# Performance work log

Hardware: AMD Instinct MI355X
Metric: run time of the kernel (lower is better)

Reference implementation:

```python
import math
import jax, jax.numpy as jnp
import numpy as np

N_NODES = 20000
N_EDGES = 320000
N_GRAPHS = 50
MAX_RADIUS = 3.5
NB = 8
NUM_NEIGHBORS = 16.0
NUM_NODES_TYP = 400.0
EPS = 1e-6
C_S = math.sin(math.pi / 8)
C_X = math.cos(math.pi / 8)
SQRT3 = math.sqrt(3.0)


def silu(x):
    return x * jax.nn.sigmoid(x)


def setup_inputs() -> dict:
    key = jax.random.key(0)
    ks = jax.random.split(key, 32)
    nrm = lambda i, s: jax.random.normal(ks[i], s, dtype=jnp.float32)
    return {
        'pos': nrm(0, (N_NODES, 3)),
        'atom_type': jax.random.randint(ks[1], (N_NODES,), 0, 20),
        'edge_src': jax.random.randint(ks[2], (N_EDGES,), 0, N_NODES),
        'edge_dst': jax.random.randint(ks[3], (N_EDGES,), 0, N_NODES),
        'batch': jnp.sort(jax.random.randint(ks[4], (N_NODES,), 0, N_GRAPHS)),
        'embed': nrm(5, (20, 8)),
        'w_tp0': nrm(6, (8, 8, 8)),
        'tpself_ss': nrm(7, (2, 64, 64, 64)),
        'tpself_vv': nrm(8, (2, 32, 32, 64)),
        'tpself_sv': nrm(9, (2, 64, 32, 32)),
        'tpself_vs': nrm(10, (2, 32, 64, 32)),
        'w_pen_ss': nrm(11, (64, 64, 16)),
        'w_pen_vv': nrm(12, (32, 32, 16)),
        'w_last': nrm(13, (16, 16, 1)),
        'sc0': nrm(14, (8, 96)),
        'lin1_0': nrm(15, (8, 8)),
        'fc0_w1': nrm(16, (NB, 64)),
        'fc0_w2': nrm(17, (64, 16)),
        'lin2_0s': nrm(18, (8, 96)),
        'lin2_0v': nrm(19, (8, 32)),
        'sc_s': nrm(20, (2, 64, 96)),
        'sc_v': nrm(21, (2, 32, 32)),
        'lin1_s': nrm(22, (2, 64, 64)),
        'lin1_v': nrm(23, (2, 32, 32)),
        'fc_w1': nrm(24, (2, NB, 64)),
        'fc_w2': nrm(25, (2, 64, 192)),
        'lin2_s': nrm(26, (2, 96, 96)),
        'lin2_v': nrm(27, (2, 96, 32)),
    }


def _edge_geometry(pos, edge_src, edge_dst):
    vec = pos[edge_src] - pos[edge_dst]            # [E,3]
    r = jnp.sqrt(jnp.sum(vec * vec, -1) + 1e-12)   # [E]
    r_safe = jnp.maximum(r, EPS)
    unit = vec / r_safe[:, None]
    sh0 = jnp.ones((vec.shape[0], 1), vec.dtype)   # Y_0 (component norm)
    sh1 = SQRT3 * unit                             # Y_1 (component norm)
    u = 2.0 * (r / MAX_RADIUS - 1.0)               # smooth_cutoff
    cut = 0.5 * (1.0 - jnp.cos(math.pi * u))
    cut = jnp.where(u > 0, 0.0, jnp.where(u < -1, 1.0, cut))
    ea_s = cut[:, None] * sh0
    ea_v = cut[:, None] * sh1
    n = jnp.arange(1, NB + 1, dtype=vec.dtype)     # bessel basis * sqrt(NB)
    basis = math.sqrt(2.0 / MAX_RADIUS) * jnp.sin(n[None] * math.pi * r_safe[:, None] / MAX_RADIUS) / r_safe[:, None]
    basis = basis * math.sqrt(NB)
    return ea_s, ea_v, basis


def _radial(basis, w1, w2):
    h = silu(basis @ w1 / math.sqrt(basis.shape[-1]))
    return h @ w2 / math.sqrt(w1.shape[-1])


def _tvnorm(ys, yv):
    ys = ys / jnp.sqrt(jnp.mean(ys * ys, -1, keepdims=True) + EPS)
    vn = jnp.mean(jnp.sum(yv * yv, -1), -1)
    return ys, yv / jnp.sqrt(vn + EPS)[:, None, None]


def _gate(ys, yv):
    return silu(ys[:, :64]), jax.nn.sigmoid(ys[:, 64:96])[:, :, None] * yv


def _tp_hidden(s, v, Wss, Wvv, Wsv, Wvs):
    a_s = 1.0 / math.sqrt(64 * 64 + 32 * 32)
    out_s = a_s * (jnp.einsum('ni,nj,ijk->nk', s, s, Wss)
                   + jnp.einsum('nic,njc,ijk->nk', v, v, Wvv) / SQRT3)
    a_v = 1.0 / math.sqrt(64 * 32 + 32 * 64)
    out_v = a_v * (jnp.einsum('ni,njc,ijk->nkc', s, v, Wsv)
                   + jnp.einsum('nic,nj,ijk->nkc', v, s, Wvs))
    return out_s, out_v


def _forward(pos, embed, w_tp0, tpself_ss, tpself_vv, tpself_sv, tpself_vs,
             w_pen_ss, w_pen_vv, w_last, sc0, lin1_0, fc0_w1, fc0_w2,
             lin2_0s, lin2_0v, sc_s, sc_v, lin1_s, lin1_v, fc_w1, fc_w2,
             lin2_s, lin2_v, atom_type, edge_src, edge_dst, batch):
    ea_s, ea_v, basis = _edge_geometry(pos, edge_src, edge_dst)
    inv_nn = 1.0 / math.sqrt(NUM_NEIGHBORS)

    x = embed[atom_type]                                    # [N,8]
    x = jnp.einsum('ni,nj,ijk->nk', x, x, w_tp0) / 8.0      # tp_self[0]

    # layer 0 convolution: 8x0e -> 96x0e + 32x1o
    sc_scal = x @ sc0 / math.sqrt(8)
    xl = x @ lin1_0 / math.sqrt(8)
    w = _radial(basis, fc0_w1, fc0_w2)                      # [E,16]
    xe = xl[edge_src]
    msg_s = w[:, :8] * xe * ea_s                            # 0e x 0e -> 0e
    msg_v = (w[:, 8:] * xe)[:, :, None] * ea_v[:, None, :]  # 0e x 1o -> 1o
    agg_s = jax.ops.segment_sum(msg_s, edge_dst, N_NODES) * inv_nn
    agg_v = jax.ops.segment_sum(msg_v, edge_dst, N_NODES) * inv_nn
    ys = C_S * sc_scal + C_X * (agg_s @ lin2_0s / math.sqrt(8))
    yv = jnp.einsum('nuc,uk->nkc', agg_v, lin2_0v) / math.sqrt(8)  # sc mask=0 here
    ys, yv = _tvnorm(ys, yv)
    s, v = _gate(ys, yv)                                    # [N,64],[N,32,3]

    # layers 1,2: residual with self tensor product
    for i in range(2):
        scs = s @ sc_s[i] / math.sqrt(64)
        scv = jnp.einsum('nuc,uk->nkc', v, sc_v[i]) / math.sqrt(32)
        ls = s @ lin1_s[i] / math.sqrt(64)
        lv = jnp.einsum('nuc,uk->nkc', v, lin1_v[i]) / math.sqrt(32)
        w = _radial(basis, fc_w1[i], fc_w2[i])              # [E,192]
        se, ve = ls[edge_src], lv[edge_src]
        m0 = w[:, :64] * se * ea_s                                    # 0e x 0e -> 0e
        m3 = w[:, 160:] * (jnp.sum(ve * ea_v[:, None, :], -1) / SQRT3)  # 1o x 1o -> 0e
        m1 = (w[:, 64:128] * se)[:, :, None] * ea_v[:, None, :]      # 0e x 1o -> 1o
        m2 = w[:, 128:160, None] * ve * ea_s[:, :, None]             # 1o x 0e -> 1o
        agg_s = jax.ops.segment_sum(jnp.concatenate([m0, m3], 1), edge_dst, N_NODES) * inv_nn
        agg_v = jax.ops.segment_sum(jnp.concatenate([m1, m2], 1), edge_dst, N_NODES) * inv_nn
        ys = C_S * scs + C_X * (agg_s @ lin2_s[i] / math.sqrt(96))
        yv = C_S * scv + C_X * (jnp.einsum('nuc,uk->nkc', agg_v, lin2_v[i]) / math.sqrt(96))
        ys, yv = _tvnorm(ys, yv)
        gs, gv = _gate(ys, yv)
        gs, gv = _tp_hidden(gs, gv, tpself_ss[i], tpself_vv[i], tpself_sv[i], tpself_vs[i])
        s = s + 0.1 * gs
        v = v + 0.1 * gv

    a_pen = 1.0 / math.sqrt(64 * 64 + 32 * 32)
    x16 = a_pen * (jnp.einsum('ni,nj,ijk->nk', s, s, w_pen_ss)
                   + jnp.einsum('nic,njc,ijk->nk', v, v, w_pen_vv) / SQRT3)
    x16 = silu(x16)
    out = jnp.einsum('ni,nj,ijo->no', x16, x16, w_last) / 16.0
    return jax.ops.segment_sum(out, batch, N_GRAPHS) / math.sqrt(NUM_NODES_TYP)


def reference(pos, embed, w_tp0, tpself_ss, tpself_vv, tpself_sv, tpself_vs,
              w_pen_ss, w_pen_vv, w_last, sc0, lin1_0, fc0_w1, fc0_w2,
              lin2_0s, lin2_0v, sc_s, sc_v, lin1_s, lin1_v, fc_w1, fc_w2,
              lin2_s, lin2_v, atom_type, edge_src, edge_dst, batch):
    return _forward(pos, embed, w_tp0, tpself_ss, tpself_vv, tpself_sv, tpself_vs,
                    w_pen_ss, w_pen_vv, w_last, sc0, lin1_0, fc0_w1, fc0_w2,
                    lin2_0s, lin2_0v, sc_s, sc_v, lin1_s, lin1_v, fc_w1, fc_w2,
                    lin2_s, lin2_v, atom_type, edge_src, edge_dst, batch)
```

## Files before the change

kernel.cpp:

```cpp
#include <hip/hip_runtime.h>
#include <math.h>

#define NN 20000
#define NE 320000
#define NG 50

#define INV_SQRT8  0.35355339059327373f
#define INV_SQRT32 0.17677669529663687f
#define INV_SQRT96 0.10206207261596575f
#define INV_NN     0.25f
#define CS_        0.3826834323650898f
#define CX_        0.9238795325112867f
#define SQRT3_     1.7320508075688772f
#define INV_SQRT3  0.5773502691896258f
#define A_S_       0.013975424859373686f
#define A_V_       0.015625f
#define PI_        3.14159265358979323846f

typedef __attribute__((ext_vector_type(8))) short bf16x8;
typedef __attribute__((ext_vector_type(4))) float f32x4;

__device__ __forceinline__ float siluf(float x) { return x / (1.0f + expf(-x)); }
__device__ __forceinline__ float sigmf(float x) { return 1.0f / (1.0f + expf(-x)); }

__device__ __forceinline__ void bsplit(float x, unsigned short& h, unsigned short& l) {
  unsigned int u = __float_as_uint(x);
  unsigned short hh = (unsigned short)((u + 0x7FFFu + ((u>>16)&1u))>>16);
  float fh = __uint_as_float(((unsigned int)hh)<<16);
  float r = x - fh;
  unsigned int u2 = __float_as_uint(r);
  unsigned short ll = (unsigned short)((u2 + 0x7FFFu + ((u2>>16)&1u))>>16);
  h = hh; l = ll;
}

__global__ __launch_bounds__(256) void k_hist(const int* __restrict__ edst, int* __restrict__ deg) {
  int e = blockIdx.x*256 + threadIdx.x;
  if (e < NE) atomicAdd(&deg[edst[e]], 1);
}

__global__ __launch_bounds__(256) void k_scan(const int* __restrict__ deg,
                                              int* __restrict__ rows, int* __restrict__ cursor) {
  __shared__ int buf[256];
  __shared__ int carry;
  int t = threadIdx.x;
  if (t == 0) { carry = 0; rows[0] = 0; }
  __syncthreads();
  for (int base = 0; base < NN; base += 256) {
    int i = base + t;
    int v = (i < NN) ? deg[i] : 0;
    buf[t] = v; __syncthreads();
    #pragma unroll
    for (int off = 1; off < 256; off <<= 1) {
      int x = (t >= off) ? buf[t-off] : 0;
      __syncthreads();
      buf[t] += x;
      __syncthreads();
    }
    int incl = buf[t] + carry;
    if (i < NN) { rows[i+1] = incl; cursor[i] = incl - v; }
    __syncthreads();
    if (t == 255) carry = incl;
    __syncthreads();
  }
}

__global__ __launch_bounds__(256) void k_scatter(const int* __restrict__ edst,
                                                 int* __restrict__ cursor, int* __restrict__ perm) {
  int e = blockIdx.x*256 + threadIdx.x;
  if (e >= NE) return;
  int p = atomicAdd(&cursor[edst[e]], 1);
  perm[p] = e;
}

__global__ __launch_bounds__(256) void k_geom(
    const float* __restrict__ pos, const int* __restrict__ esrc, const int* __restrict__ edst,
    const int* __restrict__ perm, int* __restrict__ esrc_s,
    float* __restrict__ ea_s, float* __restrict__ ea_v, float* __restrict__ basis) {
  int p = blockIdx.x*256 + threadIdx.x;
  if (p >= NE) return;
  int e = perm[p];
  int s = esrc[e], d = edst[e];
  esrc_s[p] = s;
  float vx = pos[3*s]   - pos[3*d];
  float vy = pos[3*s+1] - pos[3*d+1];
  float vz = pos[3*s+2] - pos[3*d+2];
  float r  = sqrtf(vx*vx + vy*vy + vz*vz + 1e-12f);
  float rs = fmaxf(r, 1e-6f);
  float inv = 1.0f / rs;
  float u = 2.0f*(r*(1.0f/3.5f) - 1.0f);
  float cut;
  if (u > 0.0f) cut = 0.0f;
  else if (u < -1.0f) cut = 1.0f;
  else cut = 0.5f*(1.0f - cosf(PI_*u));
  ea_s[p] = cut;
  float f = cut * SQRT3_ * inv;
  ea_v[p] = f*vx; ea_v[NE+p] = f*vy; ea_v[2*NE+p] = f*vz;
  const float cb = 2.1380899352993947f;
  #pragma unroll
  for (int n = 1; n <= 8; ++n)
    basis[(size_t)(n-1)*NE + p] = cb * sinf((float)n * (PI_/3.5f) * rs) * inv;
}

__global__ __launch_bounds__(256) void k_prep(
    const float* __restrict__ fc0_w1, const float* __restrict__ fc_w1,
    float* __restrict__ w1t) {
  int t = threadIdx.x;
  for (int idx = t; idx < 512; idx += 256) { int j = idx >> 3, k = idx & 7; w1t[idx] = fc0_w1[k*64 + j]; }
  for (int L = 0; L < 2; ++L)
    for (int idx = t; idx < 512; idx += 256) { int j = idx >> 3, k = idx & 7; w1t[512 + L*512 + idx] = fc_w1[L*512 + k*64 + j]; }
}

__global__ __launch_bounds__(256) void k_packw(
    const float* __restrict__ srcA, const float* __restrict__ srcB,
    unsigned short* __restrict__ dh, unsigned short* __restrict__ dl,
    int K, int N, int bound, float scA, float scB) {
  int idx = blockIdx.x*256 + threadIdx.x;
  if (idx >= K*N) return;
  int e = idx & 7;
  int lane = (idx >> 3) & 63;
  int rest = idx >> 9;
  int NT = N >> 4;
  int nt = rest % NT;
  int kt = rest / NT;
  int k = kt*32 + (lane>>4)*8 + e;
  int n = nt*16 + (lane&15);
  float w;
  if (k < bound) w = srcA[(size_t)k*N + n]*scA;
  else           w = srcB[(size_t)(k-bound)*N + n]*scB;
  unsigned short h, l;
  bsplit(w, h, l);
  dh[idx] = h; dl[idx] = l;
}

__global__ __launch_bounds__(256) void k_node0(
    const int* __restrict__ atype, const float* __restrict__ embed,
    const float* __restrict__ w_tp0, const float* __restrict__ sc0, const float* __restrict__ lin1_0,
    float* __restrict__ SC, float* __restrict__ LSB0) {
  int n = blockIdx.x*256 + threadIdx.x;
  if (n >= NN) return;
  int at = atype[n];
  float x[8];
  #pragma unroll
  for (int i = 0; i < 8; ++i) x[i] = embed[at*8 + i];
  float tc[8] = {0,0,0,0,0,0,0,0};
  #pragma unroll
  for (int i = 0; i < 8; ++i)
    #pragma unroll
    for (int j = 0; j < 8; ++j) {
      float p = x[i]*x[j];
      #pragma unroll
      for (int k = 0; k < 8; ++k) tc[k] += p * w_tp0[(i*8+j)*8 + k];
    }
  #pragma unroll
  for (int k = 0; k < 8; ++k) tc[k] *= 0.125f;
  #pragma unroll 1
  for (int k = 0; k < 96; ++k) {
    float a = 0.f;
    #pragma unroll
    for (int i = 0; i < 8; ++i) a += tc[i]*sc0[i*96+k];
    SC[(size_t)k*NN + n] = a * INV_SQRT8;
  }
  #pragma unroll
  for (int u = 0; u < 8; ++u) {
    float a = 0.f;
    #pragma unroll
    for (int i = 0; i < 8; ++i) a += tc[i]*lin1_0[i*8+u];
    LSB0[(size_t)n*8 + u] = a * INV_SQRT8;
  }
}

__global__ __launch_bounds__(256) void k_radial0(
    const float* __restrict__ BAS, const float* __restrict__ EAS,
    const float* __restrict__ w1t, const float* __restrict__ w2,
    float* __restrict__ RW, int pLo, int pHi, int cap) {
  __shared__ float tile[256*17];
  int t = threadIdx.x;
  int idx = blockIdx.x*256 + t;
  int p = pLo + idx;
  bool alive = p < pHi;
  float h[64];
  float es = 0.f;
  if (alive) {
    float b[8];
    #pragma unroll
    for (int k = 0; k < 8; ++k) b[k] = BAS[(size_t)k*NE + p];
    #pragma unroll
    for (int j = 0; j < 64; ++j) {
      float a = 0.f;
      #pragma unroll
      for (int k = 0; k < 8; ++k) a += b[k]*w1t[j*8+k];
      h[j] = siluf(a * INV_SQRT8);
    }
    es = EAS[p];
  }
  if (alive) {
    float acc[16] = {};
    #pragma unroll
    for (int j = 0; j < 64; ++j) {
      float hj = h[j];
      #pragma unroll
      for (int c = 0; c < 16; ++c) acc[c] += hj * w2[j*16 + c];
    }
    #pragma unroll
    for (int c = 0; c < 16; ++c) {
      float a = acc[c] * 0.125f;
      if (c < 8) a *= es;
      tile[t*17 + c] = a;
    }
  }
  __syncthreads();
  int e0 = blockIdx.x*256;
  #pragma unroll
  for (int i = 0; i < 16; ++i) {
    int lin = i*256 + t;
    int e = lin >> 4, c = lin & 15;
    if (pLo + e0 + e < pHi)
      RW[(size_t)(e0 + e)*16 + c] = tile[e*17 + c];
  }
}

__global__ __launch_bounds__(256) void k_radial(
    const float* __restrict__ BAS, const float* __restrict__ EAS,
    const float* __restrict__ w1t, const float* __restrict__ w2,
    float* __restrict__ RW, int pLo, int pHi, int cap) {
  __shared__ float tile[256*17];
  int t = threadIdx.x;
  int idx = blockIdx.x*256 + t;
  int p = pLo + idx;
  bool alive = p < pHi;
  float h[64];
  float es = 0.f;
  if (alive) {
    float b[8];
    #pragma unroll
    for (int k = 0; k < 8; ++k) b[k] = BAS[(size_t)k*NE + p];
    #pragma unroll
    for (int j = 0; j < 64; ++j) {
      float a = 0.f;
      #pragma unroll
      for (int k = 0; k < 8; ++k) a += b[k]*w1t[j*8+k];
      h[j] = siluf(a * INV_SQRT8);
    }
    es = EAS[p];
  }
  int e0 = blockIdx.x*256;
  int cc0 = blockIdx.y*3;
  #pragma unroll 1
  for (int ci = 0; ci < 3; ++ci) {
    int cc = cc0 + ci;
    if (alive) {
      float acc[16] = {};
      #pragma unroll
      for (int j = 0; j < 64; ++j) {
        float hj = h[j];
        const float* wr = w2 + j*192 + cc*16;
        #pragma unroll
        for (int c = 0; c < 16; ++c) acc[c] += hj * wr[c];
      }
      #pragma unroll
      for (int c = 0; c < 16; ++c) {
        int ch = cc*16 + c;
        float a = acc[c] * 0.125f;
        float f = (ch < 64) ? es : ((ch < 128) ? 1.0f : ((ch < 160) ? es : INV_SQRT3));
        tile[t*17 + c] = a*f;
      }
    }
    __syncthreads();
    #pragma unroll
    for (int i = 0; i < 16; ++i) {
      int lin = i*256 + t;
      int e = lin >> 4, c = lin & 15;
      if (pLo + e0 + e < pHi)
        RW[(size_t)(e0 + e)*192 + cc*16 + c] = tile[e*17 + c];
    }
    __syncthreads();
  }
}

__global__ __launch_bounds__(256) void k_gather0(
    const int* __restrict__ rows, const int* __restrict__ esrc_s,
    const float* __restrict__ EAV, const float* __restrict__ RW,
    const float* __restrict__ LSB0, float* __restrict__ AG0,
    int pLo, int pHi, int cap) {
  int t = blockIdx.x*256 + threadIdx.x;
  int d = t >> 3, u = t & 7;
  int lo = rows[d], hi = rows[d+1];
  lo = lo > pLo ? lo : pLo;
  hi = hi < pHi ? hi : pHi;
  if (lo >= hi) return;
  float aS = 0.f, a0 = 0.f, a1 = 0.f, a2 = 0.f;
  for (int p = lo; p < hi; ++p) {
    int q = p - pLo;
    int sn = esrc_s[p];
    float xe = LSB0[(size_t)sn*8 + u];
    const float* rwp = RW + (size_t)q*16;
    float r0 = rwp[u];
    float r1 = rwp[8+u];
    aS += r0*xe;
    float tt = r1*xe;
    a0 += tt*EAV[p]; a1 += tt*EAV[NE+p]; a2 += tt*EAV[2*NE+p];
  }
  float* ag = AG0 + (size_t)d*32;
  ag[u] += aS;
  ag[8 + u*3 + 0] += a0;
  ag[8 + u*3 + 1] += a1;
  ag[8 + u*3 + 2] += a2;
}

__global__ __launch_bounds__(256) void k_gather(
    const int* __restrict__ rows, const int* __restrict__ esrc_s,
    const float* __restrict__ EAS, const float* __restrict__ EAV,
    const float* __restrict__ RW, const float* __restrict__ LSB, const float* __restrict__ LVB,
    float* __restrict__ AG, int pLo, int pHi, int cap) {
  int gw = (blockIdx.x*256 + threadIdx.x) >> 6;
  int lane = threadIdx.x & 63;
  if (gw >= NN) return;
  int lo = rows[gw], hi = rows[gw+1];
  lo = lo > pLo ? lo : pLo;
  hi = hi < pHi ? hi : pHi;
  if (lo >= hi) return;
  int k = lane & 31;
  bool low = lane < 32;
  float aS=0.f, aV0=0.f, aV1=0.f, aV2=0.f, aS2=0.f, aW0=0.f, aW1=0.f, aW2=0.f;
  for (int p = lo; p < hi; ++p) {
    int q = p - pLo;
    int sn = esrc_s[p];
    float ev0 = EAV[p], ev1 = EAV[NE+p], ev2 = EAV[2*NE+p];
    float se = LSB[(size_t)sn*64 + lane];
    const float* rwp = RW + (size_t)q*192;
    float r0 = rwp[lane];
    float r1 = rwp[64+lane];
    aS += r0*se;
    float t = r1*se;
    aV0 += t*ev0; aV1 += t*ev1; aV2 += t*ev2;
    if (low) {
      float ve0 = LVB[(size_t)sn*96 + k*3 + 0];
      float ve1 = LVB[(size_t)sn*96 + k*3 + 1];
      float ve2 = LVB[(size_t)sn*96 + k*3 + 2];
      float r2 = rwp[128+k];
      float r3 = rwp[160+k];
      aS2 += r3*(ve0*ev0 + ve1*ev1 + ve2*ev2);
      aW0 += r2*ve0; aW1 += r2*ve1; aW2 += r2*ve2;
    }
  }
  float* ag = AG + (size_t)gw*384;
  ag[lane] += aS;
  ag[96 + lane*3 + 0] += aV0;
  ag[96 + lane*3 + 1] += aV1;
  ag[96 + lane*3 + 2] += aV2;
  if (low) {
    ag[64 + k] += aS2;
    ag[96 + (64+k)*3 + 0] += aW0;
    ag[96 + (64+k)*3 + 1] += aW1;
    ag[96 + (64+k)*3 + 2] += aW2;
  }
}

__global__ __launch_bounds__(256) void k_upd0(
    const float* __restrict__ lin2_0s, const float* __restrict__ lin2_0v,
    float* __restrict__ SC, float* __restrict__ SCV,
    const float* __restrict__ AG0,
    float* __restrict__ SB, float* __restrict__ VB) {
  int n = blockIdx.x*256 + threadIdx.x;
  if (n >= NN) return;
  float as[8], av[24];
  #pragma unroll
  for (int u = 0; u < 8; ++u) as[u] = AG0[(size_t)n*32 + u] * INV_NN;
  #pragma unroll
  for (int u = 0; u < 24; ++u) av[u] = AG0[(size_t)n*32 + 8 + u] * INV_NN;
  float ssum = 0.f;
  #pragma unroll 1
  for (int k = 0; k < 96; ++k) {
    float a = 0.f;
    #pragma unroll
    for (int u = 0; u < 8; ++u) a += as[u]*lin2_0s[u*96+k];
    float y = CS_*SC[(size_t)k*NN+n] + CX_*INV_SQRT8*a;
    SC[(size_t)k*NN+n] = y; ssum += y*y;
  }
  float vsum = 0.f;
  #pragma unroll 1
  for (int k = 0; k < 32; ++k) {
    #pragma unroll
    for (int c = 0; c < 3; ++c) {
      float a = 0.f;
      #pragma unroll
      for (int u = 0; u < 8; ++u) a += av[u*3+c]*lin2_0v[u*32+k];
      float y = a * INV_SQRT8;
      SCV[(size_t)(k*3+c)*NN+n] = y; vsum += y*y;
    }
  }
  float sinv = rsqrtf(ssum*(1.0f/96.0f) + 1e-6f);
  float vinv = rsqrtf(vsum*(1.0f/32.0f) + 1e-6f);
  #pragma unroll 1
  for (int k = 0; k < 64; ++k) {
    float y = SC[(size_t)k*NN+n]*sinv;
    SB[(size_t)k*NN+n] = siluf(y);
  }
  #pragma unroll
  for (int k = 0; k < 32; ++k) {
    float g = sigmf(SC[(size_t)(64+k)*NN+n]*sinv) * vinv;
    #pragma unroll
    for (int c = 0; c < 3; ++c)
      VB[(size_t)(k*3+c)*NN+n] = g * SCV[(size_t)(k*3+c)*NN+n];
  }
}

__global__ __launch_bounds__(256) void k_pre(
    const float* __restrict__ scsW, const float* __restrict__ scvW,
    const float* __restrict__ l1sW, const float* __restrict__ l1vW,
    const float* __restrict__ SB, const float* __restrict__ VB,
    float* __restrict__ SC, float* __restrict__ SCV,
    float* __restrict__ LSB, float* __restrict__ LVB) {
  int n = blockIdx.x*256 + threadIdx.x;
  if (n >= NN) return;
  float s[64];
  #pragma unroll
  for (int u = 0; u < 64; ++u) s[u] = SB[(size_t)u*NN + n];
  #pragma unroll 1
  for (int k = 0; k < 96; ++k) {
    float a = 0.f;
    #pragma unroll
    for (int u = 0; u < 64; ++u) a += s[u]*scsW[u*96+k];
    SC[(size_t)k*NN+n] = a * 0.125f;
  }
  #pragma unroll 1
  for (int k = 0; k < 64; ++k) {
    float a = 0.f;
    #pragma unroll
    for (int u = 0; u < 64; ++u) a += s[u]*l1sW[u*64+k];
    LSB[(size_t)n*64 + k] = a * 0.125f;
  }
  for (int c = 0; c < 3; ++c) {
    float v[32];
    #pragma unroll
    for (int u = 0; u < 32; ++u) v[u] = VB[(size_t)(u*3+c)*NN + n];
    #pragma unroll 1
    for (int k = 0; k < 32; ++k) {
      float a = 0.f;
      #pragma unroll
      for (int u = 0; u < 32; ++u) a += v[u]*scvW[u*32+k];
      SCV[(size_t)(k*3+c)*NN+n] = a * INV_SQRT32;
    }
    #pragma unroll 1
    for (int k = 0; k < 32; ++k) {
      float a = 0.f;
      #pragma unroll
      for (int u = 0; u < 32; ++u) a += v[u]*l1vW[u*32+k];
      LVB[(size_t)n*96 + k*3 + c] = a * INV_SQRT32;
    }
  }
}

__global__ __launch_bounds__(256) void k_upd(
    const float* __restrict__ l2sW, const float* __restrict__ l2vW,
    float* __restrict__ SC, float* __restrict__ SCV,
    const float* __restrict__ AG) {
  int n = blockIdx.x*256 + threadIdx.x;
  if (n >= NN) return;
  float ssum = 0.f;
  {
    float ag[96];
    #pragma unroll
    for (int u = 0; u < 96; ++u) ag[u] = AG[(size_t)n*384 + u] * INV_NN;
    #pragma unroll 1
    for (int k = 0; k < 96; ++k) {
      float a = 0.f;
      #pragma unroll
      for (int u = 0; u < 96; ++u) a += ag[u]*l2sW[u*96+k];
      float y = CS_*SC[(size_t)k*NN+n] + CX_*INV_SQRT96*a;
      SC[(size_t)k*NN+n] = y; ssum += y*y;
    }
  }
  float vsum = 0.f;
  for (int c = 0; c < 3; ++c) {
    float ag[96];
    #pragma unroll
    for (int u = 0; u < 96; ++u) ag[u] = AG[(size_t)n*384 + 96 + u*3 + c] * INV_NN;
    #pragma unroll 1
    for (int k = 0; k < 32; ++k) {
      float a = 0.f;
      #pragma unroll
      for (int u = 0; u < 96; ++u) a += ag[u]*l2vW[u*32+k];
      float y = CS_*SCV[(size_t)(k*3+c)*NN+n] + CX_*INV_SQRT96*a;
      SCV[(size_t)(k*3+c)*NN+n] = y; vsum += y*y;
    }
  }
  float sinv = rsqrtf(ssum*(1.0f/96.0f) + 1e-6f);
  float vinv = rsqrtf(vsum*(1.0f/32.0f) + 1e-6f);
  #pragma unroll 1
  for (int k = 0; k < 64; ++k) {
    float y = SC[(size_t)k*NN+n]*sinv;
    SC[(size_t)k*NN+n] = siluf(y);
  }
  #pragma unroll
  for (int k = 0; k < 32; ++k) {
    float g = sigmf(SC[(size_t)(64+k)*NN+n]*sinv) * vinv;
    #pragma unroll
    for (int c = 0; c < 3; ++c)
      SCV[(size_t)(k*3+c)*NN+n] *= g;
  }
}

template<int MODE>
__global__ __launch_bounds__(256) void k_tpg(
    const unsigned short* __restrict__ WH, const unsigned short* __restrict__ WL,
    const float* __restrict__ S, const float* __restrict__ V,
    float* __restrict__ DST) {
  constexpr int K   = (MODE==1) ? 4096 : 5120;
  constexpr int NT  = (MODE==0) ? 4 : ((MODE==1) ? 2 : 1);
  constexpr int BND = (MODE==1) ? 2048 : 4096;
  constexpr int NSTEP = K/32;
  __shared__ float s_lds[32][68];
  __shared__ float v_lds[(MODE==1)?1:3][32][36];
  __shared__ unsigned short ph[2][64][8];
  __shared__ unsigned short pl[2][64][8];
  int t = threadIdx.x;
  int nb = blockIdx.x*32;
  int c  = (MODE==1) ? blockIdx.y : 0;
  for (int idx = t; idx < 32*64; idx += 256) {
    int m = idx & 31, ch = idx >> 5;
    s_lds[m][ch] = S[(size_t)ch*NN + nb + m];
  }
  if (MODE == 1) {
    for (int idx = t; idx < 32*32; idx += 256) {
      int m = idx & 31, kch = idx >> 5;
      v_lds[0][m][kch] = V[(size_t)(kch*3 + c)*NN + nb + m];
    }
  } else {
    for (int idx = t; idx < 32*96; idx += 256) {
      int m = idx & 31, rest = idx >> 5;
      int cc = rest % 3, kch = rest / 3;
      v_lds[cc][m][kch] = V[(size_t)rest*NN + nb + m];
    }
  }
  __syncthreads();
  int wv = t >> 6, lane = t & 63;
  int bms   = t >> 7;
  int bu    = t & 127;
  int bfl   = bu >> 1;
  int bhalf = bu & 1;
  int bm    = bms*16 + (bfl&15);
  int bkl   = (bfl>>4)*8 + bhalf*4;
  int my_nt = (MODE==0) ? wv : ((MODE==1) ? (wv&1) : 0);
  f32x4 accA = {0.f,0.f,0.f,0.f};
  f32x4 accB = {0.f,0.f,0.f,0.f};
  for (int kt = 0; kt < NSTEP; ++kt) {
    size_t boff = (((size_t)kt*NT + my_nt)*64 + lane)*8;
    bf16x8 bh = *reinterpret_cast<const bf16x8*>(WH + boff);
    bf16x8 bl = *reinterpret_cast<const bf16x8*>(WL + boff);
    int k0 = kt*32 + bkl;
    float p0, p1, p2, p3;
    if (MODE != 1) {
      if (k0 < BND) {
        int i = k0 >> 6, j0 = k0 & 63;
        float si = s_lds[bm][i];
        p0 = si*s_lds[bm][j0+0]; p1 = si*s_lds[bm][j0+1];
        p2 = si*s_lds[bm][j0+2]; p3 = si*s_lds[bm][j0+3];
      } else {
        int kk = k0 - BND;
        int i = kk >> 5, j0 = kk & 31;
        float a0 = v_lds[0][bm][i], a1 = v_lds[1][bm][i], a2 = v_lds[2][bm][i];
        p0 = a0*v_lds[0][bm][j0+0] + a1*v_lds[1][bm][j0+0] + a2*v_lds[2][bm][j0+0];
        p1 = a0*v_lds[0][bm][j0+1] + a1*v_lds[1][bm][j0+1] + a2*v_lds[2][bm][j0+1];
        p2 = a0*v_lds[0][bm][j0+2] + a1*v_lds[1][bm][j0+2] + a2*v_lds[2][bm][j0+2];
        p3 = a0*v_lds[0][bm][j0+3] + a1*v_lds[1][bm][j0+3] + a2*v_lds[2][bm][j0+3];
      }
    } else {
      if (k0 < BND) {
        int i = k0 >> 5, j0 = k0 & 31;
        float si = s_lds[bm][i];
        p0 = si*v_lds[0][bm][j0+0]; p1 = si*v_lds[0][bm][j0+1];
        p2 = si*v_lds[0][bm][j0+2]; p3 = si*v_lds[0][bm][j0+3];
      } else {
        int kk = k0 - BND;
        int i = kk >> 6, j0 = kk & 63;
        float vi = v_lds[0][bm][i];
        p0 = vi*s_lds[bm][j0+0]; p1 = vi*s_lds[bm][j0+1];
        p2 = vi*s_lds[bm][j0+2]; p3 = vi*s_lds[bm][j0+3];
      }
    }
    ushort4 hh, ll;
    bsplit(p0, hh.x, ll.x); bsplit(p1, hh.y, ll.y);
    bsplit(p2, hh.z, ll.z); bsplit(p3, hh.w, ll.w);
    *reinterpret_cast<ushort4*>(&ph[bms][bfl][bhalf*4]) = hh;
    *reinterpret_cast<ushort4*>(&pl[bms][bfl][bhalf*4]) = ll;
    __syncthreads();
    if (MODE == 0) {
      bf16x8 a0h = *reinterpret_cast<const bf16x8*>(&ph[0][lane][0]);
      bf16x8 a0l = *reinterpret_cast<const bf16x8*>(&pl[0][lane][0]);
      bf16x8 a1h = *reinterpret_cast<const bf16x8*>(&ph[1][lane][0]);
      bf16x8 a1l = *reinterpret_cast<const bf16x8*>(&pl[1][lane][0]);
      accA = __builtin_amdgcn_mfma_f32_16x16x32_bf16(a0h, bh, accA, 0, 0, 0);
      accA = __builtin_amdgcn_mfma_f32_16x16x32_bf16(a0h, bl, accA, 0, 0, 0);
      accA = __builtin_amdgcn_mfma_f32_16x16x32_bf16(a0l, bh, accA, 0, 0, 0);
      accB = __builtin_amdgcn_mfma_f32_16x16x32_bf16(a1h, bh, accB, 0, 0, 0);
      accB = __builtin_amdgcn_mfma_f32_16x16x32_bf16(a1h, bl, accB, 0, 0, 0);
      accB = __builtin_amdgcn_mfma_f32_16x16x32_bf16(a1l, bh, accB, 0, 0, 0);
    } else if (MODE == 1) {
      int ms = wv >> 1;
      bf16x8 ah = *reinterpret_cast<const bf16x8*>(&ph[ms][lane][0]);
      bf16x8 al = *reinterpret_cast<const bf16x8*>(&pl[ms][lane][0]);
      accA = __builtin_amdgcn_mfma_f32_16x16x32_bf16(ah, bh, accA, 0, 0, 0);
      accA = __builtin_amdgcn_mfma_f32_16x16x32_bf16(ah, bl, accA, 0, 0, 0);
      accA = __builtin_amdgcn_mfma_f32_16x16x32_bf16(al, bh, accA, 0, 0, 0);
    } else {
      if (wv < 2) {
        bf16x8 ah = *reinterpret_cast<const bf16x8*>(&ph[wv][lane][0]);
        bf16x8 al = *reinterpret_cast<const bf16x8*>(&pl[wv][lane][0]);
        accA = __builtin_amdgcn_mfma_f32_16x16x32_bf16(ah, bh, accA, 0, 0, 0);
        accA = __builtin_amdgcn_mfma_f32_16x16x32_bf16(ah, bl, accA, 0, 0, 0);
        accA = __builtin_amdgcn_mfma_f32_16x16x32_bf16(al, bh, accA, 0, 0, 0);
      }
    }
    __syncthreads();
  }
  int col = lane & 15;
  int rb  = (lane >> 4) * 4;
  if (MODE == 0) {
    #pragma unroll
    for (int r = 0; r < 4; ++r) {
      int node = nb + rb + r;
      int ch = wv*16 + col;
      DST[(size_t)ch*NN + node]      += accA[r];
      DST[(size_t)ch*NN + node + 16] += accB[r];
    }
  } else if (MODE == 1) {
    int ms = wv >> 1, ntl = wv & 1;
    #pragma unroll
    for (int r = 0; r < 4; ++r) {
      int node = nb + ms*16 + rb + r;
      int ch = ntl*16 + col;
      DST[(size_t)(ch*3 + c)*NN + node] += accA[r];
    }
  } else {
    if (wv < 2) {
      #pragma unroll
      for (int r = 0; r < 4; ++r) {
        int node = nb + wv*16 + rb + r;
        DST[(size_t)col*NN + node] = accA[r];
      }
    }
  }
}

__global__ __launch_bounds__(256) void k_fin2(
    const float* __restrict__ wl, const int* __restrict__ batch,
    const float* __restrict__ X16, float* __restrict__ out) {
  __shared__ float bins[NG];
  int t = threadIdx.x;
  for (int i = t; i < NG; i += 256) bins[i] = 0.f;
  __syncthreads();
  int n = blockIdx.x*256 + t;
  if (n < NN) {
    float x16[16];
    #pragma unroll
    for (int k = 0; k < 16; ++k) x16[k] = siluf(X16[(size_t)k*NN + n]);
    float o = 0.f;
    #pragma unroll
    for (int i = 0; i < 16; ++i) {
      float xi = x16[i];
      #pragma unroll
      for (int j = 0; j < 16; ++j) o += xi*x16[j]*wl[i*16+j];
    }
    o *= (1.0f/16.0f)*0.05f;
    atomicAdd(&bins[batch[n]], o);
  }
  __syncthreads();
  for (int i = t; i < NG; i += 256)
    if (bins[i] != 0.f) atomicAdd(&out[i], bins[i]);
}

extern "C" void kernel_launch(void* const* d_in, const int* in_sizes, int n_in,
                              void* d_out, int out_size, void* d_ws, size_t ws_size,
                              hipStream_t stream) {
  const float* pos     = (const float*)d_in[0];
  const int*   atype   = (const int*)d_in[1];
  const int*   esrc    = (const int*)d_in[2];
  const int*   edst    = (const int*)d_in[3];
  const int*   batch   = (const int*)d_in[4];
  const float* embed   = (const float*)d_in[5];
  const float* w_tp0   = (const float*)d_in[6];
  const float* tpss    = (const float*)d_in[7];
  const float* tpvv    = (const float*)d_in[8];
  const float* tpsv    = (const float*)d_in[9];
  const float* tpvs    = (const float*)d_in[10];
  const float* pen_ss  = (const float*)d_in[11];
  const float* pen_vv  = (const float*)d_in[12];
  const float* w_last  = (const float*)d_in[13];
  const float* sc0     = (const float*)d_in[14];
  const float* lin1_0  = (const float*)d_in[15];
  const float* fc0_w1  = (const float*)d_in[16];
  const float* fc0_w2  = (const float*)d_in[17];
  const float* lin2_0s = (const float*)d_in[18];
  const float* lin2_0v = (const float*)d_in[19];
  const float* sc_s    = (const float*)d_in[20];
  const float* sc_v    = (const float*)d_in[21];
  const float* lin1_s  = (const float*)d_in[22];
  const float* lin1_v  = (const float*)d_in[23];
  const float* fc_w1   = (const float*)d_in[24];
  const float* fc_w2   = (const float*)d_in[25];
  const float* lin2_s  = (const float*)d_in[26];
  const float* lin2_v  = (const float*)d_in[27];

  float* ws = (float*)d_ws;
  float* out = (float*)d_out;

  size_t o = 0;
  float* EA_S = ws + o; o += NE;
  float* EA_V = ws + o; o += 3*(size_t)NE;
  float* BAS  = ws + o; o += 8*(size_t)NE;
  float* W1T  = ws + o; o += 1536;
  float* SC   = ws + o; o += 96*(size_t)NN;
  float* SCV  = ws + o; o += 96*(size_t)NN;
  float* LSB  = ws + o; o += 64*(size_t)NN;
  float* LVB  = ws + o; o += 96*(size_t)NN;
  float* AG   = ws + o; o += 384*(size_t)NN;
  float* AG0  = ws + o; o += 32*(size_t)NN;
  float* SB   = ws + o; o += 64*(size_t)NN;
  float* VB   = ws + o; o += 96*(size_t)NN;
  float* X16  = ws + o; o += 16*(size_t)NN;
  int* ESRC_S = (int*)(ws + o); o += NE;
  int* PERM   = (int*)(ws + o); o += NE;
  int* DEG    = (int*)(ws + o); o += NN;
  int* ROWS   = (int*)(ws + o); o += NN + 1;
  int* CURSOR = (int*)(ws + o); o += NN;
  unsigned short* PWS = (unsigned short*)(ws + o); o += 999424;
  unsigned short* WSh[2] = { PWS,            PWS + 655360 };
  unsigned short* WSl[2] = { PWS + 327680,   PWS + 983040 };
  unsigned short* WVh[2] = { PWS + 1310720,  PWS + 1572864 };
  unsigned short* WVl[2] = { PWS + 1441792,  PWS + 1703936 };
  unsigned short* WPh    =   PWS + 1835008;
  unsigned short* WPl    =   PWS + 1916928;
  float* RW   = ws + o;

  size_t availF = (ws_size/4 > o) ? (ws_size/4 - o) : 0;
  size_t capL = (availF/192) & ~(size_t)255;
  int cap  = (int)(capL < (size_t)NE ? capL : (size_t)NE);
  if (cap < 1024) cap = 1024;
  size_t cap0L = (availF/16) & ~(size_t)255;
  int cap0 = (int)(cap0L < (size_t)NE ? cap0L : (size_t)NE);
  if (cap0 < 1024) cap0 = 1024;

  const int nbE = NE/256;
  const int nbN = (NN+255)/256;
  const int nbG = NN*64/256;
  const int nbG0 = NN*8/256;
  const int nbM = NN/32;

  hipMemsetAsync(out, 0, NG*sizeof(float), stream);
  hipMemsetAsync(DEG, 0, NN*sizeof(int), stream);
  k_hist<<<nbE,256,0,stream>>>(edst, DEG);
  k_scan<<<1,256,0,stream>>>(DEG, ROWS, CURSOR);
  k_scatter<<<nbE,256,0,stream>>>(edst, CURSOR, PERM);
  k_geom<<<nbE,256,0,stream>>>(pos, esrc, edst, PERM, ESRC_S, EA_S, EA_V, BAS);
  k_prep<<<1,256,0,stream>>>(fc0_w1, fc_w1, W1T);
  for (int L = 0; L < 2; ++L) {
    k_packw<<<1280,256,0,stream>>>(tpss + (size_t)L*262144, tpvv + (size_t)L*65536,
                                   WSh[L], WSl[L], 5120, 64, 4096,
                                   0.1f*A_S_, 0.1f*A_S_*INV_SQRT3);
    k_packw<<<512,256,0,stream>>>(tpsv + (size_t)L*65536, tpvs + (size_t)L*65536,
                                  WVh[L], WVl[L], 4096, 32, 2048,
                                  0.1f*A_V_, 0.1f*A_V_);
  }
  k_packw<<<320,256,0,stream>>>(pen_ss, pen_vv, WPh, WPl, 5120, 16, 4096,
                                A_S_, A_S_*INV_SQRT3);
  k_node0<<<nbN,256,0,stream>>>(atype, embed, w_tp0, sc0, lin1_0, SC, LSB);

  hipMemsetAsync(AG0, 0, 32*(size_t)NN*sizeof(float), stream);
  for (int pLo = 0; pLo < NE; pLo += cap0) {
    int pHi = pLo + cap0 < NE ? pLo + cap0 : NE;
    int nb = (pHi - pLo + 255)/256;
    k_radial0<<<nb,256,0,stream>>>(BAS, EA_S, W1T, fc0_w2, RW, pLo, pHi, cap0);
    k_gather0<<<nbG0,256,0,stream>>>(ROWS, ESRC_S, EA_V, RW, LSB, AG0, pLo, pHi, cap0);
  }
  k_upd0<<<nbN,256,0,stream>>>(lin2_0s, lin2_0v, SC, SCV, AG0, SB, VB);

  for (int L = 0; L < 2; ++L) {
    k_pre<<<nbN,256,0,stream>>>(sc_s + L*64*96, sc_v + L*32*32,
                                lin1_s + L*64*64, lin1_v + L*32*32,
                                SB, VB, SC, SCV, LSB, LVB);
    hipMemsetAsync(AG, 0, 384*(size_t)NN*sizeof(float), stream);
    for (int pLo = 0; pLo < NE; pLo += cap) {
      int pHi = pLo + cap < NE ? pLo + cap : NE;
      int nb = (pHi - pLo + 255)/256;
      k_radial<<<dim3(nb,4),256,0,stream>>>(BAS, EA_S, W1T + 512 + L*512, fc_w2 + (size_t)L*12288, RW, pLo, pHi, cap);
      k_gather<<<nbG,256,0,stream>>>(ROWS, ESRC_S, EA_S, EA_V, RW, LSB, LVB, AG, pLo, pHi, cap);
    }
    k_upd<<<nbN,256,0,stream>>>(lin2_s + L*96*96, lin2_v + L*96*32, SC, SCV, AG);
    k_tpg<0><<<nbM,256,0,stream>>>(WSh[L], WSl[L], SC, SCV, SB);
    k_tpg<1><<<dim3(nbM,3),256,0,stream>>>(WVh[L], WVl[L], SC, SCV, VB);
  }
  k_tpg<2><<<nbM,256,0,stream>>>(WPh, WPl, SB, VB, X16);
  k_fin2<<<nbN,256,0,stream>>>(w_last, batch, X16, out);
}
```

Measured before the change: 2.183 ms.

## Compute per-edge radial MLP second layer with split-bf16 MFMA

Replaces the scalar FP32 per-edge radial network kernel, which recomputed the 64-wide hidden layer in each of four y-blocks, with an MFMA kernel. Each block handles 32 edges: it computes the hidden activations once, splits them into hi/lo bf16 in LDS, and multiplies by prepacked hi/lo bf16 weights using three MFMAs per tile to keep near-FP32 accuracy. A new pack kernel pre-scales fc_w2 into MFMA layout. The output stores write RW directly without the LDS transpose, so the write pattern changes.

Result: faster. 1.801 ms (-17.5%).

```diff
diff --git a/kernel.cpp b/kernel.cpp
--- a/kernel.cpp
+++ b/kernel.cpp
@@ -132,6 +132,23 @@
   dh[idx] = h; dl[idx] = l;
 }
 
+__global__ __launch_bounds__(256) void k_packr(
+    const float* __restrict__ src,
+    unsigned short* __restrict__ dh, unsigned short* __restrict__ dl) {
+  int idx = blockIdx.x*256 + threadIdx.x;
+  if (idx >= 12288) return;
+  int e = idx & 7;
+  int lane = (idx >> 3) & 63;
+  int rest = idx >> 9;
+  int nt = rest % 12, kt = rest / 12;
+  int k = kt*32 + (lane>>4)*8 + e;
+  int n = nt*16 + (lane&15);
+  float w = src[k*192 + n] * 0.125f;
+  if (n >= 160) w *= INV_SQRT3;
+  unsigned short h, l; bsplit(w, h, l);
+  dh[idx] = h; dl[idx] = l;
+}
+
 __global__ __launch_bounds__(256) void k_node0(
     const int* __restrict__ atype, const float* __restrict__ embed,
     const float* __restrict__ w_tp0, const float* __restrict__ sc0, const float* __restrict__ lin1_0,
@@ -219,61 +236,98 @@
   }
 }
 
-__global__ __launch_bounds__(256) void k_radial(
+__global__ __launch_bounds__(256) void k_radialg(
     const float* __restrict__ BAS, const float* __restrict__ EAS,
-    const float* __restrict__ w1t, const float* __restrict__ w2,
+    const float* __restrict__ w1t,
+    const unsigned short* __restrict__ WH, const unsigned short* __restrict__ WL,
     float* __restrict__ RW, int pLo, int pHi, int cap) {
-  __shared__ float tile[256*17];
+  __shared__ float bas_lds[32][9];
+  __shared__ float es_lds[32];
+  __shared__ unsigned short ph[2][2][64][8];
+  __shared__ unsigned short pl[2][2][64][8];
   int t = threadIdx.x;
-  int idx = blockIdx.x*256 + t;
-  int p = pLo + idx;
-  bool alive = p < pHi;
-  float h[64];
-  float es = 0.f;
-  if (alive) {
-    float b[8];
-    #pragma unroll
-    for (int k = 0; k < 8; ++k) b[k] = BAS[(size_t)k*NE + p];
-    #pragma unroll
-    for (int j = 0; j < 64; ++j) {
-      float a = 0.f;
-      #pragma unroll
-      for (int k = 0; k < 8; ++k) a += b[k]*w1t[j*8+k];
-      h[j] = siluf(a * INV_SQRT8);
-    }
-    es = EAS[p];
-  }
-  int e0 = blockIdx.x*256;
-  int cc0 = blockIdx.y*3;
-  #pragma unroll 1
+  int e0 = blockIdx.x*32;
+  for (int idx = t; idx < 32*8; idx += 256) {
+    int m = idx >> 3, k = idx & 7;
+    int p = pLo + e0 + m;
+    bas_lds[m][k] = (p < pHi) ? BAS[(size_t)k*NE + p] : 0.f;
+  }
+  if (t < 32) {
+    int p = pLo + e0 + t;
+    es_lds[t] = (p < pHi) ? EAS[p] : 0.f;
+  }
+  __syncthreads();
+  int bms = t >> 7, bu = t & 127, bfl = bu >> 1, bhalf = bu & 1;
+  int bm = bms*16 + (bfl & 15);
+  int jb = (bfl >> 4)*8 + bhalf*4;
+  float b0=bas_lds[bm][0],b1=bas_lds[bm][1],b2=bas_lds[bm][2],b3=bas_lds[bm][3];
+  float b4=bas_lds[bm][4],b5=bas_lds[bm][5],b6=bas_lds[bm][6],b7=bas_lds[bm][7];
+  #pragma unroll
+  for (int kt = 0; kt < 2; ++kt) {
+    ushort4 hh, ll;
+    #pragma unroll
+    for (int q = 0; q < 4; ++q) {
+      int j = kt*32 + jb + q;
+      const float* wr = w1t + j*8;
+      float a = b0*wr[0]+b1*wr[1]+b2*wr[2]+b3*wr[3]+b4*wr[4]+b5*wr[5]+b6*wr[6]+b7*wr[7];
+      float hv = siluf(a * INV_SQRT8);
+      unsigned short hq, lq; bsplit(hv, hq, lq);
+      ((unsigned short*)&hh)[q] = hq; ((unsigned short*)&ll)[q] = lq;
+    }
+    *reinterpret_cast<ushort4*>(&ph[kt][bms][bfl][bhalf*4]) = hh;
+    *reinterpret_cast<ushort4*>(&pl[kt][bms][bfl][bhalf*4]) = ll;
+  }
+  __syncthreads();
+  int wv = t >> 6, lane = t & 63;
+  f32x4 accA0 = {0.f,0.f,0.f,0.f}, accA1 = {0.f,0.f,0.f,0.f}, accA2 = {0.f,0.f,0.f,0.f};
+  f32x4 accB0 = {0.f,0.f,0.f,0.f}, accB1 = {0.f,0.f,0.f,0.f}, accB2 = {0.f,0.f,0.f,0.f};
+  #pragma unroll
+  for (int kt = 0; kt < 2; ++kt) {
+    bf16x8 a0h = *reinterpret_cast<const bf16x8*>(&ph[kt][0][lane][0]);
+    bf16x8 a0l = *reinterpret_cast<const bf16x8*>(&pl[kt][0][lane][0]);
+    bf16x8 a1h = *reinterpret_cast<const bf16x8*>(&ph[kt][1][lane][0]);
+    bf16x8 a1l = *reinterpret_cast<const bf16x8*>(&pl[kt][1][lane][0]);
+    #pragma unroll
+    for (int ci = 0; ci < 3; ++ci) {
+      int nt = wv*3 + ci;
+      size_t boff = (((size_t)kt*12 + nt)*64 + lane)*8;
+      bf16x8 bh = *reinterpret_cast<const bf16x8*>(WH + boff);
+      bf16x8 bl = *reinterpret_cast<const bf16x8*>(WL + boff);
+      f32x4 aA = (ci==0)?accA0:((ci==1)?accA1:accA2);
+      f32x4 aB = (ci==0)?accB0:((ci==1)?accB1:accB2);
+      aA = __builtin_amdgcn_mfma_f32_16x16x32_bf16(a0h, bh, aA, 0,0,0);
+      aA = __builtin_amdgcn_mfma_f32_16x16x32_bf16(a0h, bl, aA, 0,0,0);
+      aA = __builtin_amdgcn_mfma_f32_16x16x32_bf16(a0l, bh, aA, 0,0,0);
+      aB = __builtin_amdgcn_mfma_f32_16x16x32_bf16(a1h, bh, aB, 0,0,0);
+      aB = __builtin_amdgcn_mfma_f32_16x16x32_bf16(a1h, bl, aB, 0,0,0);
+      aB = __builtin_amdgcn_mfma_f32_16x16x32_bf16(a1l, bh, aB, 0,0,0);
+      if (ci==0) { accA0 = aA; accB0 = aB; }
+      else if (ci==1) { accA1 = aA; accB1 = aB; }
+      else { accA2 = aA; accB2 = aB; }
+    }
+  }
+  int col = lane & 15, rb = (lane>>4)*4;
+  #pragma unroll
   for (int ci = 0; ci < 3; ++ci) {
-    int cc = cc0 + ci;
-    if (alive) {
-      float acc[16] = {};
-      #pragma unroll
-      for (int j = 0; j < 64; ++j) {
-        float hj = h[j];
-        const float* wr = w2 + j*192 + cc*16;
-        #pragma unroll
-        for (int c = 0; c < 16; ++c) acc[c] += hj * wr[c];
+    int ch = (wv*3+ci)*16 + col;
+    bool esf = (ch < 64) || (ch >= 128 && ch < 160);
+    f32x4 aA = (ci==0)?accA0:((ci==1)?accA1:accA2);
+    f32x4 aB = (ci==0)?accB0:((ci==1)?accB1:accB2);
+    #pragma unroll
+    for (int r = 0; r < 4; ++r) {
+      int m0 = rb + r;
+      if (pLo + e0 + m0 < pHi) {
+        float v = aA[r];
+        if (esf) v *= es_lds[m0];
+        RW[(size_t)(e0 + m0)*192 + ch] = v;
       }
-      #pragma unroll
-      for (int c = 0; c < 16; ++c) {
-        int ch = cc*16 + c;
-        float a = acc[c] * 0.125f;
-        float f = (ch < 64) ? es : ((ch < 128) ? 1.0f : ((ch < 160) ? es : INV_SQRT3));
-        tile[t*17 + c] = a*f;
+      int m1 = 16 + rb + r;
+      if (pLo + e0 + m1 < pHi) {
+        float v = aB[r];
+        if (esf) v *= es_lds[m1];
+        RW[(size_t)(e0 + m1)*192 + ch] = v;
       }
     }
-    __syncthreads();
-    #pragma unroll
-    for (int i = 0; i < 16; ++i) {
-      int lin = i*256 + t;
-      int e = lin >> 4, c = lin & 15;
-      if (pLo + e0 + e < pHi)
-        RW[(size_t)(e0 + e)*192 + cc*16 + c] = tile[e*17 + c];
-    }
-    __syncthreads();
   }
 }
 
@@ -731,6 +785,9 @@
   unsigned short* WVl[2] = { PWS + 1441792,  PWS + 1703936 };
   unsigned short* WPh    =   PWS + 1835008;
   unsigned short* WPl    =   PWS + 1916928;
+  unsigned short* PRW = (unsigned short*)(ws + o); o += 24576;
+  unsigned short* WRh[2] = { PRW,           PRW + 24576 };
+  unsigned short* WRl[2] = { PRW + 12288,   PRW + 36864 };
   float* RW   = ws + o;
 
   size_t availF = (ws_size/4 > o) ? (ws_size/4 - o) : 0;
@@ -761,6 +818,7 @@
     k_packw<<<512,256,0,stream>>>(tpsv + (size_t)L*65536, tpvs + (size_t)L*65536,
                                   WVh[L], WVl[L], 4096, 32, 2048,
                                   0.1f*A_V_, 0.1f*A_V_);
+    k_packr<<<48,256,0,stream>>>(fc_w2 + (size_t)L*12288, WRh[L], WRl[L]);
   }
   k_packw<<<320,256,0,stream>>>(pen_ss, pen_vv, WPh, WPl, 5120, 16, 4096,
                                 A_S_, A_S_*INV_SQRT3);
@@ -782,8 +840,9 @@
     hipMemsetAsync(AG, 0, 384*(size_t)NN*sizeof(float), stream);
     for (int pLo = 0; pLo < NE; pLo += cap) {
       int pHi = pLo + cap < NE ? pLo + cap : NE;
-      int nb = (pHi - pLo + 255)/256;
-      k_radial<<<dim3(nb,4),256,0,stream>>>(BAS, EA_S, W1T + 512 + L*512, fc_w2 + (size_t)L*12288, RW, pLo, pHi, cap);
+      int nb32 = (pHi - pLo + 31)/32;
+      k_radialg<<<nb32,256,0,stream>>>(BAS, EA_S, W1T + 512 + L*512, WRh[L], WRl[L],
+                                       RW, pLo, pHi, cap);
       k_gather<<<nbG,256,0,stream>>>(ROWS, ESRC_S, EA_S, EA_V, RW, LSB, LVB, AG, pLo, pHi, cap);
     }
     k_upd<<<nbN,256,0,stream>>>(lin2_s + L*96*96, lin2_v + L*96*32, SC, SCV, AG);
```
